# Optimization experiments

Hardware: AMD Instinct MI355X
Metric: run time of the kernel (lower is better)

The kernel has to match this reference:

```python
import jax, jax.numpy as jnp
import numpy as np

D_MODEL = 1024
N_HEADS = 16
D_K = D_MODEL // N_HEADS
B, S = 4, 2048


def setup_inputs() -> dict:
    key = jax.random.key(0)
    ks = jax.random.split(key, 12)
    s = 1.0 / np.sqrt(D_MODEL)
    inp = {
        "Q": jax.random.normal(ks[0], (B, S, D_MODEL), jnp.float32),
        "K": jax.random.normal(ks[1], (B, S, D_MODEL), jnp.float32),
        "V": jax.random.normal(ks[2], (B, S, D_MODEL), jnp.float32),
        "attn_mask": jax.random.randint(ks[3], (B, S, S), 0, 2, jnp.int32),
        "Wq": jax.random.normal(ks[4], (D_MODEL, D_MODEL), jnp.float32) * s,
        "bq": jnp.zeros((D_MODEL,), jnp.float32),
        "Wk": jax.random.normal(ks[5], (D_MODEL, D_MODEL), jnp.float32) * s,
        "bk": jnp.zeros((D_MODEL,), jnp.float32),
        "Wv": jax.random.normal(ks[6], (D_MODEL, D_MODEL), jnp.float32) * s,
        "bv": jnp.zeros((D_MODEL,), jnp.float32),
        "Wo": jax.random.normal(ks[7], (D_MODEL, D_MODEL), jnp.float32) * s,
        "bo": jnp.zeros((D_MODEL,), jnp.float32),
        "ln_g": jnp.ones((D_MODEL,), jnp.float32),
        "ln_b": jnp.zeros((D_MODEL,), jnp.float32),
    }
    return inp


def reference(Q, K, V, attn_mask, Wq, bq, Wk, bk, Wv, bv, Wo, bo, ln_g, ln_b):
    b = Q.shape[0]
    # QKV projections -> [b, heads, seq, d_k]
    def proj(x, W, bias):
        y = x @ W.T + bias
        return y.reshape(b, -1, N_HEADS, D_K).transpose(0, 2, 1, 3)
    q = proj(Q, Wq, bq)
    k = proj(K, Wk, bk)
    v = proj(V, Wv, bv)
    scores = jnp.einsum("bhqd,bhkd->bhqk", q, k) / np.sqrt(D_K)
    mask = attn_mask[:, None, :, :]  # broadcast over heads
    scores = jnp.where(mask == 0, jnp.float32(-1e9), scores)
    attn = jax.nn.softmax(scores, axis=-1)
    context = jnp.einsum("bhqk,bhkd->bhqd", attn, v)
    context = context.transpose(0, 2, 1, 3).reshape(b, -1, N_HEADS * D_K)
    out = context @ Wo.T + bo
    x = out + Q  # residual
    mu = jnp.mean(x, axis=-1, keepdims=True)
    var = jnp.var(x, axis=-1, keepdims=True)
    y = (x - mu) / jnp.sqrt(var + 1e-5) * ln_g + ln_b
    return (y, attn)
```

## Files before the change

### kernel.cpp

```cpp
#include <hip/hip_runtime.h>
#include <hip/hip_bf16.h>
#include <cstdint>

typedef __bf16 bf16_t;
typedef __attribute__((ext_vector_type(8))) __bf16 bf16x8;
typedef __attribute__((ext_vector_type(4))) float f32x4;

#define S_LEN 2048
#define NHEADS 16
#define DK 64
#define DMODEL 1024
#define BATCH 4
#define MROWS (BATCH * S_LEN)

__device__ __forceinline__ bf16x8 ld8(const bf16_t* p) { return *(const bf16x8*)p; }

__device__ __forceinline__ bf16x8 cvt8(const float* p) {
    f32x4 a = *(const f32x4*)p;
    f32x4 b = *(const f32x4*)(p + 4);
    bf16x8 r;
    r[0] = (bf16_t)a[0]; r[1] = (bf16_t)a[1]; r[2] = (bf16_t)a[2]; r[3] = (bf16_t)a[3];
    r[4] = (bf16_t)b[0]; r[5] = (bf16_t)b[1]; r[6] = (bf16_t)b[2]; r[7] = (bf16_t)b[3];
    return r;
}

__device__ __forceinline__ void gl_lds16(const bf16_t* g, bf16_t* l) {
    __builtin_amdgcn_global_load_lds(
        (const __attribute__((address_space(1))) uint32_t*)g,
        (__attribute__((address_space(3))) uint32_t*)l, 16, 0, 0);
}

__global__ __launch_bounds__(256) void cvt_kernel(const float* __restrict__ in,
                                                  bf16_t* __restrict__ out) {
    int i = (blockIdx.x * 256 + threadIdx.x) * 8;
    *(bf16x8*)(out + i) = cvt8(in + i);
}

__global__ __launch_bounds__(256) void pack_mask_kernel(const int* __restrict__ mask,
                                                        unsigned long long* __restrict__ bits) {
    size_t idx = (size_t)blockIdx.x * 256 + threadIdx.x;
    int v = mask[idx];
    unsigned long long b = __ballot(v != 0);
    if ((threadIdx.x & 63) == 0) bits[idx >> 6] = b;
}

__global__ __launch_bounds__(256) void gemm_bt(
    const bf16_t* __restrict__ X, const bf16_t* __restrict__ W,
    const float* __restrict__ bias, bf16_t* __restrict__ Y, int mode)
{
    __shared__ bf16_t As[2][128 * 32];
    __shared__ bf16_t Bs[2][128 * 32];
    const int K = DMODEL;
    int lane = threadIdx.x & 63;
    int wave = threadIdx.x >> 6;
    int lr = lane & 15, lg = lane >> 4;
    int wr = wave >> 1, wc = wave & 1;
    int i0 = blockIdx.x * 128;
    int j0 = blockIdx.y * 128;

    const bf16_t* xg = X + (size_t)(i0 + wave * 16 + (lane >> 2)) * K + (lane & 3) * 8;
    const bf16_t* wg = W + (size_t)(j0 + wave * 16 + (lane >> 2)) * K + (lane & 3) * 8;

    f32x4 acc[4][4] = {};

    auto stage = [&](int buf, int k0) {
        #pragma unroll
        for (int r = 0; r < 2; ++r) {
            gl_lds16(xg + (size_t)(r * 64) * K + k0, &As[buf][r * 2048 + wave * 512]);
            gl_lds16(wg + (size_t)(r * 64) * K + k0, &Bs[buf][r * 2048 + wave * 512]);
        }
    };

    stage(0, 0);
    for (int t = 0; t < K / 32; ++t) {
        __syncthreads();
        if (t + 1 < K / 32) stage((t + 1) & 1, (t + 1) * 32);
        const bf16_t* ab = &As[t & 1][(wr * 64 + lr) * 32 + lg * 8];
        const bf16_t* bb = &Bs[t & 1][(wc * 64 + lr) * 32 + lg * 8];
        bf16x8 a[4], b[4];
        #pragma unroll
        for (int m = 0; m < 4; ++m) a[m] = ld8(ab + m * 16 * 32);
        #pragma unroll
        for (int n = 0; n < 4; ++n) b[n] = ld8(bb + n * 16 * 32);
        __builtin_amdgcn_s_setprio(1);
        #pragma unroll
        for (int m = 0; m < 4; ++m)
            #pragma unroll
            for (int n = 0; n < 4; ++n)
                acc[m][n] = __builtin_amdgcn_mfma_f32_16x16x32_bf16(a[m], b[n], acc[m][n], 0, 0, 0);
        __builtin_amdgcn_s_setprio(0);
    }

    #pragma unroll
    for (int n = 0; n < 4; ++n) {
        int col = j0 + wc * 64 + n * 16 + lr;
        float bv = bias[col];
        #pragma unroll
        for (int m = 0; m < 4; ++m) {
            #pragma unroll
            for (int r = 0; r < 4; ++r) {
                int row = i0 + wr * 64 + m * 16 + lg * 4 + r;
                float v = acc[m][n][r] + bv;
                size_t off;
                if (mode == 2) {
                    off = (size_t)row * DMODEL + col;
                } else {
                    int b = row >> 11, s = row & (S_LEN - 1);
                    int h = col >> 6, d = col & (DK - 1);
                    if (mode == 0) off = ((size_t)(b * NHEADS + h) * S_LEN + s) * DK + d;
                    else           off = ((size_t)(b * NHEADS + h) * DK + d) * S_LEN + s;
                }
                Y[off] = (bf16_t)v;
            }
        }
    }
}

__global__ __launch_bounds__(256) void attn_kernel(
    const bf16_t* __restrict__ qb, const bf16_t* __restrict__ kb,
    const bf16_t* __restrict__ vT, const unsigned long long* __restrict__ mbits,
    float* __restrict__ attn_out, bf16_t* __restrict__ ctx_out)
{
    __shared__ __align__(16) float psharef[4][16][68];
    int lane = threadIdx.x & 63;
    int wave = threadIdx.x >> 6;
    int lr = lane & 15, lg = lane >> 4;
    int bh = blockIdx.x >> 5;
    int b = bh >> 4, h = bh & (NHEADS - 1);
    int q0 = (blockIdx.x & 31) * 64 + wave * 16;

    const bf16_t* qp = qb + ((size_t)bh * S_LEN + q0 + lr) * DK + lg * 8;
    bf16x8 aq0 = ld8(qp), aq1 = ld8(qp + 32);

    const bf16_t* kp = kb + ((size_t)bh * S_LEN + lr) * DK + lg * 8;
    const unsigned long long* mp = mbits + ((size_t)b * S_LEN + q0 + lg * 4) * (S_LEN / 64);

    float m[4] = {-1e30f, -1e30f, -1e30f, -1e30f};
    float l[4] = {0.f, 0.f, 0.f, 0.f};

    for (int n0 = 0; n0 < S_LEN; n0 += 64) {
        f32x4 sc[4];
        __builtin_amdgcn_s_setprio(1);
        #pragma unroll
        for (int nt = 0; nt < 4; ++nt) {
            const bf16_t* kr = kp + (size_t)(n0 + nt * 16) * DK;
            f32x4 c = {0.f, 0.f, 0.f, 0.f};
            c = __builtin_amdgcn_mfma_f32_16x16x32_bf16(aq0, ld8(kr), c, 0, 0, 0);
            c = __builtin_amdgcn_mfma_f32_16x16x32_bf16(aq1, ld8(kr + 32), c, 0, 0, 0);
            sc[nt] = c;
        }
        __builtin_amdgcn_s_setprio(0);
        int w = n0 >> 6;
        #pragma unroll
        for (int r = 0; r < 4; ++r) {
            unsigned long long mw = mp[r * (S_LEN / 64) + w];
            float sv[4];
            float mx = -1e30f;
            #pragma unroll
            for (int nt = 0; nt < 4; ++nt) {
                float s = sc[nt][r] * 0.125f;
                if (!((mw >> (nt * 16 + lr)) & 1ULL)) s = -1e9f;
                sv[nt] = s;
                mx = fmaxf(mx, s);
            }
            #pragma unroll
            for (int off = 1; off < 16; off <<= 1) mx = fmaxf(mx, __shfl_xor(mx, off, 64));
            float mn = fmaxf(m[r], mx);
            float sum = 0.f;
            #pragma unroll
            for (int nt = 0; nt < 4; ++nt) sum += __expf(sv[nt] - mn);
            #pragma unroll
            for (int off = 1; off < 16; off <<= 1) sum += __shfl_xor(sum, off, 64);
            l[r] = l[r] * __expf(m[r] - mn) + sum;
            m[r] = mn;
        }
    }
    float inv_l[4];
    #pragma unroll
    for (int r = 0; r < 4; ++r) inv_l[r] = 1.f / l[r];

    f32x4 ctx[4] = {};
    size_t attn_base = ((size_t)bh * S_LEN + q0) * S_LEN;
    for (int n0 = 0; n0 < S_LEN; n0 += 64) {
        int w = n0 >> 6;
        #pragma unroll
        for (int nt = 0; nt < 4; ++nt) {
            const bf16_t* kr = kp + (size_t)(n0 + nt * 16) * DK;
            f32x4 c = {0.f, 0.f, 0.f, 0.f};
            __builtin_amdgcn_s_setprio(1);
            c = __builtin_amdgcn_mfma_f32_16x16x32_bf16(aq0, ld8(kr), c, 0, 0, 0);
            c = __builtin_amdgcn_mfma_f32_16x16x32_bf16(aq1, ld8(kr + 32), c, 0, 0, 0);
            __builtin_amdgcn_s_setprio(0);
            #pragma unroll
            for (int r = 0; r < 4; ++r) {
                unsigned long long mw = mp[r * (S_LEN / 64) + w];
                float s = c[r] * 0.125f;
                if (!((mw >> (nt * 16 + lr)) & 1ULL)) s = -1e9f;
                float p = __expf(s - m[r]) * inv_l[r];
                psharef[wave][lg * 4 + r][nt * 16 + lr] = p;
            }
        }
        #pragma unroll
        for (int j = 0; j < 4; ++j) {
            int flat = j * 64 + lane;
            int rr = flat >> 4, cc = (flat & 15) * 4;
            *(f32x4*)(attn_out + attn_base + (size_t)rr * S_LEN + n0 + cc) =
                *(const f32x4*)&psharef[wave][rr][cc];
        }
        #pragma unroll
        for (int t = 0; t < 2; ++t) {
            bf16x8 ap = cvt8(&psharef[wave][lr][t * 32 + lg * 8]);
            __builtin_amdgcn_s_setprio(1);
            #pragma unroll
            for (int dt = 0; dt < 4; ++dt) {
                const bf16_t* vr = vT + ((size_t)bh * DK + dt * 16 + lr) * S_LEN + n0 + t * 32 + lg * 8;
                ctx[dt] = __builtin_amdgcn_mfma_f32_16x16x32_bf16(ap, ld8(vr), ctx[dt], 0, 0, 0);
            }
            __builtin_amdgcn_s_setprio(0);
        }
    }
    #pragma unroll
    for (int dt = 0; dt < 4; ++dt) {
        #pragma unroll
        for (int r = 0; r < 4; ++r) {
            size_t row = (size_t)b * S_LEN + q0 + lg * 4 + r;
            int col = h * DK + dt * 16 + lr;
            ctx_out[row * DMODEL + col] = (bf16_t)ctx[dt][r];
        }
    }
}

__global__ __launch_bounds__(256) void ln_kernel(
    const bf16_t* __restrict__ proj, const float* __restrict__ Qres,
    const float* __restrict__ gamma, const float* __restrict__ beta,
    float* __restrict__ y)
{
    __shared__ float red[8];
    int row = blockIdx.x;
    int tid = threadIdx.x;
    int lane = tid & 63, wave = tid >> 6;
    const bf16_t* pr = proj + (size_t)row * DMODEL;
    const float*  qr = Qres + (size_t)row * DMODEL;
    float x[4];
    float sum = 0.f, sumsq = 0.f;
    #pragma unroll
    for (int i = 0; i < 4; ++i) {
        int c = tid + i * 256;
        float v = (float)pr[c] + qr[c];
        x[i] = v; sum += v; sumsq += v * v;
    }
    #pragma unroll
    for (int off = 1; off < 64; off <<= 1) {
        sum += __shfl_xor(sum, off, 64);
        sumsq += __shfl_xor(sumsq, off, 64);
    }
    if (lane == 0) { red[wave] = sum; red[4 + wave] = sumsq; }
    __syncthreads();
    sum = red[0] + red[1] + red[2] + red[3];
    sumsq = red[4] + red[5] + red[6] + red[7];
    float mu = sum * (1.f / DMODEL);
    float var = sumsq * (1.f / DMODEL) - mu * mu;
    float rstd = rsqrtf(var + 1e-5f);
    #pragma unroll
    for (int i = 0; i < 4; ++i) {
        int c = tid + i * 256;
        y[(size_t)row * DMODEL + c] = (x[i] - mu) * rstd * gamma[c] + beta[c];
    }
}

extern "C" void kernel_launch(void* const* d_in, const int* in_sizes, int n_in,
                              void* d_out, int out_size, void* d_ws, size_t ws_size,
                              hipStream_t stream) {
    (void)in_sizes; (void)n_in; (void)out_size; (void)ws_size;
    const float* Q   = (const float*)d_in[0];
    const float* Kin = (const float*)d_in[1];
    const float* Vin = (const float*)d_in[2];
    const int*   mask= (const int*)d_in[3];
    const float* Wq  = (const float*)d_in[4];
    const float* bq  = (const float*)d_in[5];
    const float* Wk  = (const float*)d_in[6];
    const float* bk  = (const float*)d_in[7];
    const float* Wv  = (const float*)d_in[8];
    const float* bv  = (const float*)d_in[9];
    const float* Wo  = (const float*)d_in[10];
    const float* bo  = (const float*)d_in[11];
    const float* lng = (const float*)d_in[12];
    const float* lnb = (const float*)d_in[13];

    const size_t NE = (size_t)BATCH * S_LEN * DMODEL;
    const size_t WN = (size_t)DMODEL * DMODEL;
    bf16_t* wqb  = (bf16_t*)d_ws;
    bf16_t* wkb  = wqb + WN;
    bf16_t* wvb  = wkb + WN;
    bf16_t* wob  = wvb + WN;
    bf16_t* qbuf = wob + WN;
    bf16_t* kbuf = qbuf + NE;
    bf16_t* vtbuf= kbuf + NE;
    bf16_t* ctxbuf = vtbuf + NE;
    bf16_t* outbuf = qbuf;
    unsigned long long* mbits = (unsigned long long*)(ctxbuf + NE);
    bf16_t* x16 = (bf16_t*)(mbits + (size_t)BATCH * S_LEN * (S_LEN / 64));

    float* y_out    = (float*)d_out;
    float* attn_out = y_out + NE;

    cvt_kernel<<<WN / 2048, 256, 0, stream>>>(Wq, wqb);
    cvt_kernel<<<WN / 2048, 256, 0, stream>>>(Wk, wkb);
    cvt_kernel<<<WN / 2048, 256, 0, stream>>>(Wv, wvb);
    cvt_kernel<<<WN / 2048, 256, 0, stream>>>(Wo, wob);

    const int mask_elems = BATCH * S_LEN * S_LEN;
    pack_mask_kernel<<<mask_elems / 256, 256, 0, stream>>>(mask, mbits);

    dim3 gg(MROWS / 128, DMODEL / 128);
    cvt_kernel<<<NE / 2048, 256, 0, stream>>>(Q, x16);
    gemm_bt<<<gg, 256, 0, stream>>>(x16, wqb, bq, qbuf, 0);
    cvt_kernel<<<NE / 2048, 256, 0, stream>>>(Kin, x16);
    gemm_bt<<<gg, 256, 0, stream>>>(x16, wkb, bk, kbuf, 0);
    cvt_kernel<<<NE / 2048, 256, 0, stream>>>(Vin, x16);
    gemm_bt<<<gg, 256, 0, stream>>>(x16, wvb, bv, vtbuf, 1);

    attn_kernel<<<BATCH * NHEADS * (S_LEN / 64), 256, 0, stream>>>(
        qbuf, kbuf, vtbuf, mbits, attn_out, ctxbuf);

    gemm_bt<<<gg, 256, 0, stream>>>(ctxbuf, wob, bo, outbuf, 2);

    ln_kernel<<<BATCH * S_LEN, 256, 0, stream>>>(outbuf, Q, lng, lnb, y_out);
}
```

Baseline: 2.093 ms.

## Batch QKV projections, transpose score layout for softmax stats, smaller out-proj tile

```diff
diff --git a/kernel.cpp b/kernel.cpp
--- a/kernel.cpp
+++ b/kernel.cpp
@@ -36,6 +36,15 @@
     *(bf16x8*)(out + i) = cvt8(in + i);
 }
 
+__global__ __launch_bounds__(256) void cvt3_kernel(const float* __restrict__ a,
+                                                   const float* __restrict__ b,
+                                                   const float* __restrict__ c,
+                                                   bf16_t* __restrict__ out) {
+    const float* src = blockIdx.y == 0 ? a : (blockIdx.y == 1 ? b : c);
+    size_t i = ((size_t)blockIdx.x * 256 + threadIdx.x) * 8;
+    *(bf16x8*)(out + (size_t)blockIdx.y * ((size_t)MROWS * DMODEL) + i) = cvt8(src + i);
+}
+
 __global__ __launch_bounds__(256) void pack_mask_kernel(const int* __restrict__ mask,
                                                         unsigned long long* __restrict__ bits) {
     size_t idx = (size_t)blockIdx.x * 256 + threadIdx.x;
@@ -44,47 +53,59 @@
     if ((threadIdx.x & 63) == 0) bits[idx >> 6] = b;
 }
 
+template <int TM>
 __global__ __launch_bounds__(256) void gemm_bt(
-    const bf16_t* __restrict__ X, const bf16_t* __restrict__ W,
-    const float* __restrict__ bias, bf16_t* __restrict__ Y, int mode)
+    const bf16_t* __restrict__ Xb, const bf16_t* __restrict__ Wb,
+    const float* __restrict__ bq_, const float* __restrict__ bk_,
+    const float* __restrict__ bv_, bf16_t* __restrict__ Yb, int batched)
 {
-    __shared__ bf16_t As[2][128 * 32];
+    constexpr int WM = TM / 2;
+    constexpr int MF = WM / 16;
+    __shared__ bf16_t As[2][TM * 32];
     __shared__ bf16_t Bs[2][128 * 32];
     const int K = DMODEL;
     int lane = threadIdx.x & 63;
     int wave = threadIdx.x >> 6;
     int lr = lane & 15, lg = lane >> 4;
     int wr = wave >> 1, wc = wave & 1;
-    int i0 = blockIdx.x * 128;
+    int i0 = blockIdx.x * TM;
     int j0 = blockIdx.y * 128;
+
+    int z = batched ? blockIdx.z : 0;
+    const bf16_t* X = Xb + (size_t)z * ((size_t)MROWS * DMODEL);
+    const bf16_t* W = Wb + (size_t)z * ((size_t)DMODEL * DMODEL);
+    const float* bias = (z == 0) ? bq_ : (z == 1 ? bk_ : bv_);
+    bf16_t* Y = Yb + (size_t)z * ((size_t)MROWS * DMODEL);
+    int mode = batched ? (z == 2 ? 1 : 0) : 2;
 
     const bf16_t* xg = X + (size_t)(i0 + wave * 16 + (lane >> 2)) * K + (lane & 3) * 8;
     const bf16_t* wg = W + (size_t)(j0 + wave * 16 + (lane >> 2)) * K + (lane & 3) * 8;
 
-    f32x4 acc[4][4] = {};
+    f32x4 acc[MF][4] = {};
 
     auto stage = [&](int buf, int k0) {
         #pragma unroll
-        for (int r = 0; r < 2; ++r) {
+        for (int r = 0; r < TM / 64; ++r)
             gl_lds16(xg + (size_t)(r * 64) * K + k0, &As[buf][r * 2048 + wave * 512]);
+        #pragma unroll
+        for (int r = 0; r < 2; ++r)
             gl_lds16(wg + (size_t)(r * 64) * K + k0, &Bs[buf][r * 2048 + wave * 512]);
-        }
     };
 
     stage(0, 0);
     for (int t = 0; t < K / 32; ++t) {
         __syncthreads();
         if (t + 1 < K / 32) stage((t + 1) & 1, (t + 1) * 32);
-        const bf16_t* ab = &As[t & 1][(wr * 64 + lr) * 32 + lg * 8];
+        const bf16_t* ab = &As[t & 1][(wr * WM + lr) * 32 + lg * 8];
         const bf16_t* bb = &Bs[t & 1][(wc * 64 + lr) * 32 + lg * 8];
-        bf16x8 a[4], b[4];
-        #pragma unroll
-        for (int m = 0; m < 4; ++m) a[m] = ld8(ab + m * 16 * 32);
+        bf16x8 a[MF], b[4];
+        #pragma unroll
+        for (int m = 0; m < MF; ++m) a[m] = ld8(ab + m * 16 * 32);
         #pragma unroll
         for (int n = 0; n < 4; ++n) b[n] = ld8(bb + n * 16 * 32);
         __builtin_amdgcn_s_setprio(1);
         #pragma unroll
-        for (int m = 0; m < 4; ++m)
+        for (int m = 0; m < MF; ++m)
             #pragma unroll
             for (int n = 0; n < 4; ++n)
                 acc[m][n] = __builtin_amdgcn_mfma_f32_16x16x32_bf16(a[m], b[n], acc[m][n], 0, 0, 0);
@@ -96,19 +117,19 @@
         int col = j0 + wc * 64 + n * 16 + lr;
         float bv = bias[col];
         #pragma unroll
-        for (int m = 0; m < 4; ++m) {
+        for (int m = 0; m < MF; ++m) {
             #pragma unroll
             for (int r = 0; r < 4; ++r) {
-                int row = i0 + wr * 64 + m * 16 + lg * 4 + r;
+                int row = i0 + wr * WM + m * 16 + lg * 4 + r;
                 float v = acc[m][n][r] + bv;
                 size_t off;
                 if (mode == 2) {
                     off = (size_t)row * DMODEL + col;
                 } else {
-                    int b = row >> 11, s = row & (S_LEN - 1);
+                    int b_ = row >> 11, s = row & (S_LEN - 1);
                     int h = col >> 6, d = col & (DK - 1);
-                    if (mode == 0) off = ((size_t)(b * NHEADS + h) * S_LEN + s) * DK + d;
-                    else           off = ((size_t)(b * NHEADS + h) * DK + d) * S_LEN + s;
+                    if (mode == 0) off = ((size_t)(b_ * NHEADS + h) * S_LEN + s) * DK + d;
+                    else           off = ((size_t)(b_ * NHEADS + h) * DK + d) * S_LEN + s;
                 }
                 Y[off] = (bf16_t)v;
             }
@@ -133,52 +154,52 @@
     bf16x8 aq0 = ld8(qp), aq1 = ld8(qp + 32);
 
     const bf16_t* kp = kb + ((size_t)bh * S_LEN + lr) * DK + lg * 8;
-    const unsigned long long* mp = mbits + ((size_t)b * S_LEN + q0 + lg * 4) * (S_LEN / 64);
-
-    float m[4] = {-1e30f, -1e30f, -1e30f, -1e30f};
-    float l[4] = {0.f, 0.f, 0.f, 0.f};
-
+
+    const unsigned long long* mq = mbits + ((size_t)b * S_LEN + q0 + lr) * (S_LEN / 64);
+    float m_l = -1e30f, l_l = 0.f;
     for (int n0 = 0; n0 < S_LEN; n0 += 64) {
+        unsigned long long mw = mq[n0 >> 6];
         f32x4 sc[4];
         __builtin_amdgcn_s_setprio(1);
         #pragma unroll
         for (int nt = 0; nt < 4; ++nt) {
             const bf16_t* kr = kp + (size_t)(n0 + nt * 16) * DK;
             f32x4 c = {0.f, 0.f, 0.f, 0.f};
-            c = __builtin_amdgcn_mfma_f32_16x16x32_bf16(aq0, ld8(kr), c, 0, 0, 0);
-            c = __builtin_amdgcn_mfma_f32_16x16x32_bf16(aq1, ld8(kr + 32), c, 0, 0, 0);
+            c = __builtin_amdgcn_mfma_f32_16x16x32_bf16(ld8(kr), aq0, c, 0, 0, 0);
+            c = __builtin_amdgcn_mfma_f32_16x16x32_bf16(ld8(kr + 32), aq1, c, 0, 0, 0);
             sc[nt] = c;
         }
         __builtin_amdgcn_s_setprio(0);
-        int w = n0 >> 6;
-        #pragma unroll
-        for (int r = 0; r < 4; ++r) {
-            unsigned long long mw = mp[r * (S_LEN / 64) + w];
-            float sv[4];
-            float mx = -1e30f;
-            #pragma unroll
-            for (int nt = 0; nt < 4; ++nt) {
+        float sv[16];
+        float mx = -1e30f;
+        #pragma unroll
+        for (int nt = 0; nt < 4; ++nt)
+            #pragma unroll
+            for (int r = 0; r < 4; ++r) {
                 float s = sc[nt][r] * 0.125f;
-                if (!((mw >> (nt * 16 + lr)) & 1ULL)) s = -1e9f;
-                sv[nt] = s;
+                if (!((mw >> (nt * 16 + lg * 4 + r)) & 1ULL)) s = -1e9f;
+                sv[nt * 4 + r] = s;
                 mx = fmaxf(mx, s);
             }
-            #pragma unroll
-            for (int off = 1; off < 16; off <<= 1) mx = fmaxf(mx, __shfl_xor(mx, off, 64));
-            float mn = fmaxf(m[r], mx);
-            float sum = 0.f;
-            #pragma unroll
-            for (int nt = 0; nt < 4; ++nt) sum += __expf(sv[nt] - mn);
-            #pragma unroll
-            for (int off = 1; off < 16; off <<= 1) sum += __shfl_xor(sum, off, 64);
-            l[r] = l[r] * __expf(m[r] - mn) + sum;
-            m[r] = mn;
-        }
-    }
-    float inv_l[4];
-    #pragma unroll
-    for (int r = 0; r < 4; ++r) inv_l[r] = 1.f / l[r];
-
+        mx = fmaxf(mx, __shfl_xor(mx, 16, 64));
+        mx = fmaxf(mx, __shfl_xor(mx, 32, 64));
+        float mn = fmaxf(m_l, mx);
+        float sum = 0.f;
+        #pragma unroll
+        for (int i = 0; i < 16; ++i) sum += __expf(sv[i] - mn);
+        sum += __shfl_xor(sum, 16, 64);
+        sum += __shfl_xor(sum, 32, 64);
+        l_l = l_l * __expf(m_l - mn) + sum;
+        m_l = mn;
+    }
+    float m2[4], invl[4];
+    #pragma unroll
+    for (int r = 0; r < 4; ++r) {
+        m2[r]   = __shfl(m_l, lg * 4 + r, 64);
+        invl[r] = 1.f / __shfl(l_l, lg * 4 + r, 64);
+    }
+
+    const unsigned long long* mp = mbits + ((size_t)b * S_LEN + q0 + lg * 4) * (S_LEN / 64);
     f32x4 ctx[4] = {};
     size_t attn_base = ((size_t)bh * S_LEN + q0) * S_LEN;
     for (int n0 = 0; n0 < S_LEN; n0 += 64) {
@@ -196,7 +217,7 @@
                 unsigned long long mw = mp[r * (S_LEN / 64) + w];
                 float s = c[r] * 0.125f;
                 if (!((mw >> (nt * 16 + lr)) & 1ULL)) s = -1e9f;
-                float p = __expf(s - m[r]) * inv_l[r];
+                float p = __expf(s - m2[r]) * invl[r];
                 psharef[wave][lg * 4 + r][nt * 16 + lr] = p;
             }
         }
@@ -299,10 +320,10 @@
     bf16_t* ctxbuf = vtbuf + NE;
     bf16_t* outbuf = qbuf;
     unsigned long long* mbits = (unsigned long long*)(ctxbuf + NE);
-    bf16_t* x16 = (bf16_t*)(mbits + (size_t)BATCH * S_LEN * (S_LEN / 64));
 
     float* y_out    = (float*)d_out;
     float* attn_out = y_out + NE;
+    bf16_t* x16 = (bf16_t*)attn_out;
 
     cvt_kernel<<<WN / 2048, 256, 0, stream>>>(Wq, wqb);
     cvt_kernel<<<WN / 2048, 256, 0, stream>>>(Wk, wkb);
@@ -312,18 +333,16 @@
     const int mask_elems = BATCH * S_LEN * S_LEN;
     pack_mask_kernel<<<mask_elems / 256, 256, 0, stream>>>(mask, mbits);
 
-    dim3 gg(MROWS / 128, DMODEL / 128);
-    cvt_kernel<<<NE / 2048, 256, 0, stream>>>(Q, x16);
-    gemm_bt<<<gg, 256, 0, stream>>>(x16, wqb, bq, qbuf, 0);
-    cvt_kernel<<<NE / 2048, 256, 0, stream>>>(Kin, x16);
-    gemm_bt<<<gg, 256, 0, stream>>>(x16, wkb, bk, kbuf, 0);
-    cvt_kernel<<<NE / 2048, 256, 0, stream>>>(Vin, x16);
-    gemm_bt<<<gg, 256, 0, stream>>>(x16, wvb, bv, vtbuf, 1);
+    cvt3_kernel<<<dim3(NE / 2048, 3), 256, 0, stream>>>(Q, Kin, Vin, x16);
+
+    gemm_bt<128><<<dim3(MROWS / 128, DMODEL / 128, 3), 256, 0, stream>>>(
+        x16, wqb, bq, bk, bv, qbuf, 1);
 
     attn_kernel<<<BATCH * NHEADS * (S_LEN / 64), 256, 0, stream>>>(
         qbuf, kbuf, vtbuf, mbits, attn_out, ctxbuf);
 
-    gemm_bt<<<gg, 256, 0, stream>>>(ctxbuf, wob, bo, outbuf, 2);
+    gemm_bt<64><<<dim3(MROWS / 64, DMODEL / 128), 256, 0, stream>>>(
+        ctxbuf, wob, bo, bo, bo, outbuf, 0);
 
     ln_kernel<<<BATCH * S_LEN, 256, 0, stream>>>(outbuf, Q, lng, lnb, y_out);
 }
```

Measured after the change: 2.070 ms. No clear change (-1.1%).
